# Kernel tuning notes

Hardware: AMD Instinct MI355X
Metric: run time of the kernel (lower is better)

## Reference

```python
import jax, jax.numpy as jnp
import numpy as np

B, S, D_IN, D_H = 8, 4096, 256, 512
EPS = 1e-6


def setup_inputs() -> dict:
    key = jax.random.key(0)
    ks = jax.random.split(key, 5)
    scale = 1.0 / np.sqrt(D_IN)  # torch Linear default init scale (uniform bound)
    x = jax.random.normal(ks[0], (B, S, D_IN), dtype=jnp.float32)
    Wi = jax.random.normal(ks[1], (D_IN, D_H), dtype=jnp.float32) * scale
    Wf = jax.random.normal(ks[2], (D_IN, D_H), dtype=jnp.float32) * scale
    Wo = jax.random.normal(ks[3], (D_IN, D_H), dtype=jnp.float32) * scale
    Wz = jax.random.normal(ks[4], (D_IN, D_H), dtype=jnp.float32) * scale
    zb = jnp.zeros((D_H,), dtype=jnp.float32)
    return {"x": x, "Wi": Wi, "bi": zb, "Wf": Wf, "bf": zb,
            "Wo": Wo, "bo": zb, "Wz": Wz, "bz": zb}


def _xlstm_forward(x, Wi, bi, Wf, bf, Wo, bo, Wz, bz):
    # Batched projections over all timesteps at once: [B,S,D_H] each.
    i_t = jnp.exp(jnp.clip(jnp.einsum('bsd,dh->bsh', x, Wi) + bi, -20.0, 0.0))
    f_t = jnp.exp(jnp.clip(jnp.einsum('bsd,dh->bsh', x, Wf) + bf, -20.0, 0.0))
    o_t = jax.nn.sigmoid(jnp.einsum('bsd,dh->bsh', x, Wo) + bo)
    z_t = jnp.tanh(jnp.einsum('bsd,dh->bsh', x, Wz) + bz)

    def step(carry, gates):
        c, n = carry
        i, f, o, z = gates
        c = f * c + i * z
        n = f * n + i
        h = o * (c / (n + EPS))
        return (c, n), h

    c0 = jnp.zeros((x.shape[0], Wi.shape[1]), dtype=x.dtype)
    n0 = jnp.ones((x.shape[0], Wi.shape[1]), dtype=x.dtype)
    # time-major scan over the recurrence
    gates_tm = tuple(jnp.swapaxes(g, 0, 1) for g in (i_t, f_t, o_t, z_t))  # [S,B,H]
    _, h_tm = jax.lax.scan(step, (c0, n0), gates_tm)
    return jnp.swapaxes(h_tm, 0, 1)  # [B,S,H]


def reference(x, Wi, bi, Wf, bf, Wo, bo, Wz, bz):
    return _xlstm_forward(x, Wi, bi, Wf, bf, Wo, bo, Wz, bz)
```

## Files before the change

### kernel.cpp

```cpp
#include <hip/hip_runtime.h>
#include <hip/hip_bf16.h>
#include <cstdint>
#include <cstddef>

typedef __hip_bfloat16 bf16;
typedef __attribute__((ext_vector_type(8))) short short8;
typedef __attribute__((ext_vector_type(4))) short short4v;
typedef __attribute__((ext_vector_type(4))) float floatx4;

#define BB 8
#define SS 4096
#define DIN 256
#define DH 512
#define NCH 64
#define CHUNK 64

__device__ __forceinline__ float b2f(bf16 v) { return __bfloat162float(v); }

__global__ __launch_bounds__(256) void convert_x(
    const float* __restrict__ X, bf16* __restrict__ Xb)
{
    const int idx = blockIdx.x * 256 + threadIdx.x;
    float4 v = ((const float4*)X)[idx];
    bf16 o[4] = {__float2bfloat16(v.x), __float2bfloat16(v.y),
                 __float2bfloat16(v.z), __float2bfloat16(v.w)};
    ((short4v*)Xb)[idx] = *(const short4v*)o;
}

__global__ __launch_bounds__(256) void transpose_w(
    const float* __restrict__ Wi, const float* __restrict__ Wf,
    const float* __restrict__ Wo, const float* __restrict__ Wz,
    bf16* __restrict__ Wt)
{
    int o  = blockIdx.x * 256 + threadIdx.x;
    int nf = o >> 8;
    int k  = o & 255;
    int g  = nf >> 9;
    int hh = nf & 511;
    const float* W = (g == 0) ? Wi : (g == 1) ? Wf : (g == 2) ? Wo : Wz;
    Wt[o] = __float2bfloat16(W[(size_t)k * DH + hh]);
}

__device__ __forceinline__ void load16_lds(const bf16* g, short* l)
{
    __builtin_amdgcn_global_load_lds(
        (const __attribute__((address_space(1))) unsigned int*)g,
        (__attribute__((address_space(3))) unsigned int*)l,
        16, 0, 0);
}

__global__ __launch_bounds__(256) void gemm_mfma(
    const bf16* __restrict__ Xb, const bf16* __restrict__ Wt,
    const float* __restrict__ bi, const float* __restrict__ bfv,
    const float* __restrict__ bo, const float* __restrict__ bz,
    bf16* __restrict__ Pi, bf16* __restrict__ Pf,
    float* Po , bf16* __restrict__ Pz)
{
    __shared__ __align__(16) short As[128 * 32];
    __shared__ __align__(16) short Bs[128 * 32];

    const int tid  = threadIdx.x;
    const int m0   = blockIdx.x * 128;
    const int n0   = blockIdx.y * 128;
    const int wave = tid >> 6, lane = tid & 63;
    const int wm   = (wave >> 1) * 64, wn = (wave & 1) * 64;
    const int l15  = lane & 15;
    const int q    = lane >> 4;

    floatx4 acc[4][4];
#pragma unroll
    for (int i = 0; i < 4; i++)
#pragma unroll
        for (int j = 0; j < 4; j++) acc[i][j] = (floatx4){0.f, 0.f, 0.f, 0.f};

    const int r_ld = tid >> 2;
    const int c_ld = tid & 3;
    const bf16* agp0 = Xb + (size_t)(m0 + r_ld) * DIN + c_ld * 8;
    const bf16* agp1 = Xb + (size_t)(m0 + 64 + r_ld) * DIN + c_ld * 8;
    const bf16* bgp0 = Wt + (size_t)(n0 + r_ld) * DIN + c_ld * 8;
    const bf16* bgp1 = Wt + (size_t)(n0 + 64 + r_ld) * DIN + c_ld * 8;

    for (int k0 = 0; k0 < DIN; k0 += 32) {
        load16_lds(agp0 + k0, &As[tid * 8]);
        load16_lds(agp1 + k0, &As[2048 + tid * 8]);
        load16_lds(bgp0 + k0, &Bs[tid * 8]);
        load16_lds(bgp1 + k0, &Bs[2048 + tid * 8]);
        __syncthreads();

        short8 af[4], bfr[4];
#pragma unroll
        for (int ti = 0; ti < 4; ti++)
            af[ti] = *(const short8*)&As[(wm + ti * 16 + l15) * 32 + q * 8];
#pragma unroll
        for (int tj = 0; tj < 4; tj++)
            bfr[tj] = *(const short8*)&Bs[(wn + tj * 16 + l15) * 32 + q * 8];
#pragma unroll
        for (int ti = 0; ti < 4; ti++)
#pragma unroll
            for (int tj = 0; tj < 4; tj++)
                acc[ti][tj] = __builtin_amdgcn_mfma_f32_16x16x32_bf16(
                    af[ti], bfr[tj], acc[ti][tj], 0, 0, 0);
        __syncthreads();
    }

    const int g = n0 >> 9;
    const float* bias = (g == 0) ? bi : (g == 1) ? bfv : (g == 2) ? bo : bz;
    bf16* pb = (g == 0) ? Pi : (g == 1) ? Pf : Pz;

#pragma unroll
    for (int ti = 0; ti < 4; ti++) {
        const int mrow = m0 + wm + ti * 16 + q * 4;
#pragma unroll
        for (int tj = 0; tj < 4; tj++) {
            const int n  = n0 + wn + tj * 16 + l15;
            const int hh = n & 511;
            const float bsv = bias[hh];
#pragma unroll
            for (int r = 0; r < 4; r++) {
                const float v = acc[ti][tj][r] + bsv;
                float a;
                if (g == 0 || g == 1) {
                    a = __expf(fminf(fmaxf(v, -20.f), 0.f));
                } else if (g == 2) {
                    float vc = fminf(fmaxf(v, -30.f), 30.f);
                    a = 1.f / (1.f + __expf(-vc));
                } else {
                    float vc = fminf(fmaxf(v, -30.f), 30.f);
                    a = tanhf(vc);
                }
                const size_t oidx = (size_t)(mrow + r) * DH + hh;
                if (g == 2) Po[oidx] = a;
                else        pb[oidx] = __float2bfloat16(a);
            }
        }
    }
}

__global__ __launch_bounds__(256) void scan_carry(
    const bf16* __restrict__ Pi, const bf16* __restrict__ Pf,
    const bf16* __restrict__ Pz,
    float* __restrict__ Aa, float* __restrict__ Bca, float* __restrict__ Bna,
    int nb)
{
    const int h  = blockIdx.x * 256 + threadIdx.x;
    const int b  = blockIdx.y;
    const int ch = blockIdx.z;
    const size_t base = ((size_t)(b * SS + ch * CHUNK)) * DH + h;
    const bf16* gi = Pi + base;
    const bf16* gf = Pf + base;
    const bf16* gz = Pz + base;

    float A = 1.f, Bc = 0.f, Bn = 0.f;
#pragma unroll 8
    for (int s = 0; s < CHUNK; s++) {
        const size_t o = (size_t)s * DH;
        const float f  = b2f(gf[o]);
        const float iv = b2f(gi[o]);
        const float zv = b2f(gz[o]);
        Bc = fmaf(f, Bc, iv * zv);
        Bn = fmaf(f, Bn, iv);
        A *= f;
    }
    const int cidx = (ch * nb + b) * DH + h;
    Aa[cidx] = A; Bca[cidx] = Bc; Bna[cidx] = Bn;
}

__global__ __launch_bounds__(256) void scan_chunks(
    const float* __restrict__ Aa, const float* __restrict__ Bca,
    const float* __restrict__ Bna,
    float* __restrict__ Cs, float* __restrict__ Ns, int nb)
{
    const int t = blockIdx.x * 256 + threadIdx.x;
    float c = 0.f, n = 1.f;
#pragma unroll
    for (int ch = 0; ch < NCH; ch++) {
        const int cidx = ch * (nb * DH) + t;
        Cs[cidx] = c; Ns[cidx] = n;
        const float A = Aa[cidx];
        c = fmaf(A, c, Bca[cidx]);
        n = fmaf(A, n, Bna[cidx]);
    }
}

__global__ __launch_bounds__(256) void scan_emit(
    const bf16* __restrict__ Pi, const bf16* __restrict__ Pf,
    const float* Po, const bf16* __restrict__ Pz,
    const float* __restrict__ Cs, const float* __restrict__ Ns,
    float* out, int nb)
{
    const int h  = blockIdx.x * 256 + threadIdx.x;
    const int b  = blockIdx.y;
    const int ch = blockIdx.z;
    const size_t base = ((size_t)(b * SS + ch * CHUNK)) * DH + h;
    const bf16* gi = Pi + base;
    const bf16* gf = Pf + base;
    const float* go = Po + base;
    const bf16* gz = Pz + base;
    float* op = out + base;

    const int cidx = (ch * nb + b) * DH + h;
    float c = Cs[cidx], n = Ns[cidx];
#pragma unroll 4
    for (int s = 0; s < CHUNK; s++) {
        const size_t o = (size_t)s * DH;
        const float f  = b2f(gf[o]);
        const float iv = b2f(gi[o]);
        const float ov = go[o];
        const float zv = b2f(gz[o]);
        c = fmaf(f, c, iv * zv);
        n = fmaf(f, n, iv);
        op[o] = ov * (c / (n + 1e-6f));
    }
}

extern "C" void kernel_launch(void* const* d_in, const int* in_sizes, int n_in,
                              void* d_out, int out_size, void* d_ws, size_t ws_size,
                              hipStream_t stream)
{
    const float* x   = (const float*)d_in[0];
    const float* Wi  = (const float*)d_in[1];
    const float* bi  = (const float*)d_in[2];
    const float* Wf  = (const float*)d_in[3];
    const float* bfv = (const float*)d_in[4];
    const float* Wo  = (const float*)d_in[5];
    const float* bo  = (const float*)d_in[6];
    const float* Wz  = (const float*)d_in[7];
    const float* bz  = (const float*)d_in[8];
    float* out = (float*)d_out;

    int nb = BB;
    while (nb > 1) {
        size_t need = (1u << 20)
                    + (size_t)nb * SS * DIN * 2
                    + 3 * (size_t)nb * SS * DH * 2
                    + 5 * (size_t)NCH * nb * DH * 4;
        if (need <= ws_size) break;
        nb >>= 1;
    }

    const size_t plane = (size_t)nb * SS * DH;
    bf16* Wt = (bf16*)d_ws;
    bf16* Xb = (bf16*)((char*)d_ws + (1u << 20));
    bf16* Pi = Xb + (size_t)nb * SS * DIN;
    bf16* Pf = Pi + plane;
    bf16* Pz = Pf + plane;
    float* Aa  = (float*)(Pz + plane);
    float* Bca = Aa  + (size_t)NCH * nb * DH;
    float* Bna = Bca + (size_t)NCH * nb * DH;
    float* Cs  = Bna + (size_t)NCH * nb * DH;
    float* Ns  = Cs  + (size_t)NCH * nb * DH;

    transpose_w<<<2048, 256, 0, stream>>>(Wi, Wf, Wo, Wz, Wt);

    for (int b0 = 0; b0 < BB; b0 += nb) {
        const float* Xsrc = x   + (size_t)b0 * SS * DIN;
        float*       Ob   = out + (size_t)b0 * SS * DH;
        convert_x<<<nb * 1024, 256, 0, stream>>>(Xsrc, Xb);
        gemm_mfma<<<dim3(nb * SS / 128, 16), 256, 0, stream>>>(
            Xb, Wt, bi, bfv, bo, bz, Pi, Pf, Ob, Pz);
        scan_carry<<<dim3(2, nb, NCH), 256, 0, stream>>>(
            Pi, Pf, Pz, Aa, Bca, Bna, nb);
        scan_chunks<<<2 * nb, 256, 0, stream>>>(Aa, Bca, Bna, Cs, Ns, nb);
        scan_emit<<<dim3(2, nb, NCH), 256, 0, stream>>>(
            Pi, Pf, Ob, Pz, Cs, Ns, Ob, nb);
    }
}
```

Baseline: 262.0 us.

## Store output gate as bf16 and vectorize chunked scan kernels eight channels per thread

Result: faster. 244.6 us (-6.7%).

```diff
diff --git a/kernel.cpp b/kernel.cpp
--- a/kernel.cpp
+++ b/kernel.cpp
@@ -12,10 +12,15 @@
 #define SS 4096
 #define DIN 256
 #define DH 512
-#define NCH 64
-#define CHUNK 64
+#define NCH 128
+#define CHUNK 32
 
 __device__ __forceinline__ float b2f(bf16 v) { return __bfloat162float(v); }
+__device__ __forceinline__ float sh2f(short v) {
+    unsigned int u = ((unsigned int)(unsigned short)v) << 16;
+    float f; __builtin_memcpy(&f, &u, 4); return f;
+}
+__device__ __forceinline__ float frcp(float x) { return __builtin_amdgcn_rcpf(x); }
 
 __global__ __launch_bounds__(256) void convert_x(
     const float* __restrict__ X, bf16* __restrict__ Xb)
@@ -54,7 +59,7 @@
     const float* __restrict__ bi, const float* __restrict__ bfv,
     const float* __restrict__ bo, const float* __restrict__ bz,
     bf16* __restrict__ Pi, bf16* __restrict__ Pf,
-    float* Po , bf16* __restrict__ Pz)
+    bf16* __restrict__ Po, bf16* __restrict__ Pz)
 {
     __shared__ __align__(16) short As[128 * 32];
     __shared__ __align__(16) short Bs[128 * 32];
@@ -105,15 +110,14 @@
 
     const int g = n0 >> 9;
     const float* bias = (g == 0) ? bi : (g == 1) ? bfv : (g == 2) ? bo : bz;
-    bf16* pb = (g == 0) ? Pi : (g == 1) ? Pf : Pz;
+    bf16* pb = (g == 0) ? Pi : (g == 1) ? Pf : (g == 2) ? Po : Pz;
 
 #pragma unroll
     for (int ti = 0; ti < 4; ti++) {
         const int mrow = m0 + wm + ti * 16 + q * 4;
 #pragma unroll
         for (int tj = 0; tj < 4; tj++) {
-            const int n  = n0 + wn + tj * 16 + l15;
-            const int hh = n & 511;
+            const int hh = (n0 + wn + tj * 16 + l15) & 511;
             const float bsv = bias[hh];
 #pragma unroll
             for (int r = 0; r < 4; r++) {
@@ -122,15 +126,11 @@
                 if (g == 0 || g == 1) {
                     a = __expf(fminf(fmaxf(v, -20.f), 0.f));
                 } else if (g == 2) {
-                    float vc = fminf(fmaxf(v, -30.f), 30.f);
-                    a = 1.f / (1.f + __expf(-vc));
+                    a = frcp(1.f + __expf(-v));
                 } else {
-                    float vc = fminf(fmaxf(v, -30.f), 30.f);
-                    a = tanhf(vc);
+                    a = 1.f - 2.f * frcp(__expf(2.f * v) + 1.f);
                 }
-                const size_t oidx = (size_t)(mrow + r) * DH + hh;
-                if (g == 2) Po[oidx] = a;
-                else        pb[oidx] = __float2bfloat16(a);
+                pb[(size_t)(mrow + r) * DH + hh] = __float2bfloat16(a);
             }
         }
     }
@@ -142,27 +142,39 @@
     float* __restrict__ Aa, float* __restrict__ Bca, float* __restrict__ Bna,
     int nb)
 {
-    const int h  = blockIdx.x * 256 + threadIdx.x;
-    const int b  = blockIdx.y;
-    const int ch = blockIdx.z;
-    const size_t base = ((size_t)(b * SS + ch * CHUNK)) * DH + h;
-    const bf16* gi = Pi + base;
-    const bf16* gf = Pf + base;
-    const bf16* gz = Pz + base;
-
-    float A = 1.f, Bc = 0.f, Bn = 0.f;
-#pragma unroll 8
+    const int tid = threadIdx.x;
+    const int ch  = blockIdx.x * 4 + (tid >> 6);
+    const int b   = blockIdx.y;
+    const int hg  = (tid & 63) * 8;
+    const size_t base = ((size_t)(b * SS + ch * CHUNK)) * DH + hg;
+
+    float A[8], Bc[8], Bn[8];
+#pragma unroll
+    for (int j = 0; j < 8; j++) { A[j] = 1.f; Bc[j] = 0.f; Bn[j] = 0.f; }
+
+#pragma unroll 4
     for (int s = 0; s < CHUNK; s++) {
-        const size_t o = (size_t)s * DH;
-        const float f  = b2f(gf[o]);
-        const float iv = b2f(gi[o]);
-        const float zv = b2f(gz[o]);
-        Bc = fmaf(f, Bc, iv * zv);
-        Bn = fmaf(f, Bn, iv);
-        A *= f;
-    }
-    const int cidx = (ch * nb + b) * DH + h;
-    Aa[cidx] = A; Bca[cidx] = Bc; Bna[cidx] = Bn;
+        const size_t o = base + (size_t)s * DH;
+        short8 i8 = *(const short8*)(Pi + o);
+        short8 f8 = *(const short8*)(Pf + o);
+        short8 z8 = *(const short8*)(Pz + o);
+#pragma unroll
+        for (int j = 0; j < 8; j++) {
+            const float f  = sh2f(f8[j]);
+            const float iv = sh2f(i8[j]);
+            const float zv = sh2f(z8[j]);
+            Bc[j] = fmaf(f, Bc[j], iv * zv);
+            Bn[j] = fmaf(f, Bn[j], iv);
+            A[j] *= f;
+        }
+    }
+    const size_t cidx = (size_t)(ch * nb + b) * DH + hg;
+#pragma unroll
+    for (int j = 0; j < 2; j++) {
+        *(floatx4*)(Aa  + cidx + j * 4) = *(floatx4*)&A[j * 4];
+        *(floatx4*)(Bca + cidx + j * 4) = *(floatx4*)&Bc[j * 4];
+        *(floatx4*)(Bna + cidx + j * 4) = *(floatx4*)&Bn[j * 4];
+    }
 }
 
 __global__ __launch_bounds__(256) void scan_chunks(
@@ -172,9 +184,8 @@
 {
     const int t = blockIdx.x * 256 + threadIdx.x;
     float c = 0.f, n = 1.f;
-#pragma unroll
     for (int ch = 0; ch < NCH; ch++) {
-        const int cidx = ch * (nb * DH) + t;
+        const size_t cidx = (size_t)ch * (nb * DH) + t;
         Cs[cidx] = c; Ns[cidx] = n;
         const float A = Aa[cidx];
         c = fmaf(A, c, Bca[cidx]);
@@ -184,32 +195,44 @@
 
 __global__ __launch_bounds__(256) void scan_emit(
     const bf16* __restrict__ Pi, const bf16* __restrict__ Pf,
-    const float* Po, const bf16* __restrict__ Pz,
+    const bf16* __restrict__ Po, const bf16* __restrict__ Pz,
     const float* __restrict__ Cs, const float* __restrict__ Ns,
-    float* out, int nb)
-{
-    const int h  = blockIdx.x * 256 + threadIdx.x;
-    const int b  = blockIdx.y;
-    const int ch = blockIdx.z;
-    const size_t base = ((size_t)(b * SS + ch * CHUNK)) * DH + h;
-    const bf16* gi = Pi + base;
-    const bf16* gf = Pf + base;
-    const float* go = Po + base;
-    const bf16* gz = Pz + base;
-    float* op = out + base;
-
-    const int cidx = (ch * nb + b) * DH + h;
-    float c = Cs[cidx], n = Ns[cidx];
+    float* __restrict__ out, int nb)
+{
+    const int tid = threadIdx.x;
+    const int ch  = blockIdx.x * 4 + (tid >> 6);
+    const int b   = blockIdx.y;
+    const int hg  = (tid & 63) * 8;
+    const size_t base = ((size_t)(b * SS + ch * CHUNK)) * DH + hg;
+    const size_t cidx = (size_t)(ch * nb + b) * DH + hg;
+
+    float c[8], n[8];
+#pragma unroll
+    for (int j = 0; j < 2; j++) {
+        *(floatx4*)&c[j * 4] = *(const floatx4*)(Cs + cidx + j * 4);
+        *(floatx4*)&n[j * 4] = *(const floatx4*)(Ns + cidx + j * 4);
+    }
+
 #pragma unroll 4
     for (int s = 0; s < CHUNK; s++) {
-        const size_t o = (size_t)s * DH;
-        const float f  = b2f(gf[o]);
-        const float iv = b2f(gi[o]);
-        const float ov = go[o];
-        const float zv = b2f(gz[o]);
-        c = fmaf(f, c, iv * zv);
-        n = fmaf(f, n, iv);
-        op[o] = ov * (c / (n + 1e-6f));
+        const size_t o = base + (size_t)s * DH;
+        short8 i8 = *(const short8*)(Pi + o);
+        short8 f8 = *(const short8*)(Pf + o);
+        short8 o8 = *(const short8*)(Po + o);
+        short8 z8 = *(const short8*)(Pz + o);
+        float h[8];
+#pragma unroll
+        for (int j = 0; j < 8; j++) {
+            const float f  = sh2f(f8[j]);
+            const float iv = sh2f(i8[j]);
+            const float ov = sh2f(o8[j]);
+            const float zv = sh2f(z8[j]);
+            c[j] = fmaf(f, c[j], iv * zv);
+            n[j] = fmaf(f, n[j], iv);
+            h[j] = ov * c[j] * frcp(n[j] + 1e-6f);
+        }
+        *(floatx4*)(out + o)     = *(floatx4*)&h[0];
+        *(floatx4*)(out + o + 4) = *(floatx4*)&h[4];
     }
 }
 
@@ -232,7 +255,7 @@
     while (nb > 1) {
         size_t need = (1u << 20)
                     + (size_t)nb * SS * DIN * 2
-                    + 3 * (size_t)nb * SS * DH * 2
+                    + 4 * (size_t)nb * SS * DH * 2
                     + 5 * (size_t)NCH * nb * DH * 4;
         if (need <= ws_size) break;
         nb >>= 1;
@@ -243,7 +266,8 @@
     bf16* Xb = (bf16*)((char*)d_ws + (1u << 20));
     bf16* Pi = Xb + (size_t)nb * SS * DIN;
     bf16* Pf = Pi + plane;
-    bf16* Pz = Pf + plane;
+    bf16* Po = Pf + plane;
+    bf16* Pz = Po + plane;
     float* Aa  = (float*)(Pz + plane);
     float* Bca = Aa  + (size_t)NCH * nb * DH;
     float* Bna = Bca + (size_t)NCH * nb * DH;
@@ -257,11 +281,11 @@
         float*       Ob   = out + (size_t)b0 * SS * DH;
         convert_x<<<nb * 1024, 256, 0, stream>>>(Xsrc, Xb);
         gemm_mfma<<<dim3(nb * SS / 128, 16), 256, 0, stream>>>(
-            Xb, Wt, bi, bfv, bo, bz, Pi, Pf, Ob, Pz);
-        scan_carry<<<dim3(2, nb, NCH), 256, 0, stream>>>(
+            Xb, Wt, bi, bfv, bo, bz, Pi, Pf, Po, Pz);
+        scan_carry<<<dim3(NCH / 4, nb), 256, 0, stream>>>(
             Pi, Pf, Pz, Aa, Bca, Bna, nb);
         scan_chunks<<<2 * nb, 256, 0, stream>>>(Aa, Bca, Bna, Cs, Ns, nb);
-        scan_emit<<<dim3(2, nb, NCH), 256, 0, stream>>>(
-            Pi, Pf, Ob, Pz, Cs, Ns, Ob, nb);
-    }
-}
+        scan_emit<<<dim3(NCH / 4, nb), 256, 0, stream>>>(
+            Pi, Pf, Po, Pz, Cs, Ns, Ob, nb);
+    }
+}
```
